# Kernel tuning notes

Measured on AMD Instinct MI355X. Metric: run time of the kernel, lower is better.

## Reference

```python
import jax, jax.numpy as jnp
import numpy as np

B, S, I, H = 16, 2048, 1024, 1024

def setup_inputs() -> dict:
    key = jax.random.key(0)
    ks = jax.random.split(key, 6)
    scale_ih = 1.0 / np.sqrt(I)
    scale_hh = 1.0 / np.sqrt(H)
    return {
        "x": jax.random.normal(ks[0], (B, S, I), dtype=jnp.float32),
        "hx": jax.random.normal(ks[1], (B, H), dtype=jnp.float32),
        "W_ih": jax.random.normal(ks[2], (H, I), dtype=jnp.float32) * scale_ih,
        "W_hh": jax.random.normal(ks[3], (H, H), dtype=jnp.float32) * scale_hh,
        "b_ih": jax.random.normal(ks[4], (H,), dtype=jnp.float32) * scale_ih,
        "b_hh": jax.random.normal(ks[5], (H,), dtype=jnp.float32) * scale_hh,
    }

def reference(x, hx, W_ih, W_hh, b_ih, b_hh):
    # Faithful to RecurrentCellWrapper: the Python loop passes the SAME
    # initial hx to the cell at every timestep (hx is never updated),
    # so all steps are independent and fully vectorizable.
    # cell: h' = tanh(x_t @ W_ih^T + b_ih + hx @ W_hh^T + b_hh)
    h_term = hx @ W_hh.T + b_hh + b_ih            # [B, H], shared across steps
    x_term = jnp.einsum('bsi,hi->bsh', x, W_ih)   # [B, S, H]
    out = jnp.tanh(x_term + h_term[:, None, :])   # [B, S, H]
    # batch_first=True: output already [batch, seq, hidden]
    return out
```

## Files before the change

kernel.cpp:

```cpp
#include <hip/hip_runtime.h>
#include <hip/hip_bf16.h>
#include <stdint.h>


#define M_TOT 32768
#define N_TOT 1024
#define K_TOT 1024

typedef short short8 __attribute__((ext_vector_type(8)));
typedef float f32x4  __attribute__((ext_vector_type(4)));

#define WS_XBF_OFF   0
#define WS_WBF_OFF   67108864
#define WS_HT_OFF    69206016

__device__ __forceinline__ unsigned short f32_to_bf16_rne(float f) {
    union { float f; unsigned int u; } v; v.f = f;
    unsigned int u = v.u;
    unsigned int r = u + 0x7fffu + ((u >> 16) & 1u);
    return (unsigned short)(r >> 16);
}

__device__ __forceinline__ float fast_tanh(float z) {
    float e = __expf(2.0f * z);
    return 1.0f - 2.0f / (e + 1.0f);
}

__global__ void convert_kernel(const float* __restrict__ x,
                               const float* __restrict__ wih,
                               unsigned short* __restrict__ xbf,
                               unsigned short* __restrict__ wbf) {
    const int NXV = 33554432 / 8;
    const int NWV = 1048576 / 8;
    int stride = gridDim.x * blockDim.x;
    for (int v = blockIdx.x * blockDim.x + threadIdx.x; v < NXV + NWV; v += stride) {
        const float* src; unsigned short* dst; long long base;
        if (v < NXV) { src = x;   dst = xbf; base = (long long)v * 8; }
        else         { src = wih; dst = wbf; base = (long long)(v - NXV) * 8; }
        float4 a = *(const float4*)(src + base);
        float4 b = *(const float4*)(src + base + 4);
        union { unsigned short s[8]; uint4 u; } o;
        o.s[0] = f32_to_bf16_rne(a.x); o.s[1] = f32_to_bf16_rne(a.y);
        o.s[2] = f32_to_bf16_rne(a.z); o.s[3] = f32_to_bf16_rne(a.w);
        o.s[4] = f32_to_bf16_rne(b.x); o.s[5] = f32_to_bf16_rne(b.y);
        o.s[6] = f32_to_bf16_rne(b.z); o.s[7] = f32_to_bf16_rne(b.w);
        *(uint4*)(dst + base) = o.u;
    }
}

__global__ void hterm_kernel(const float* __restrict__ hx,
                             const float* __restrict__ whh,
                             const float* __restrict__ bih,
                             const float* __restrict__ bhh,
                             float* __restrict__ ht) {
    int lane = threadIdx.x & 63;
    int w    = threadIdx.x >> 6;
    int wg   = blockIdx.x * 4 + w;
    int b = wg >> 10, h = wg & 1023;
    const float* hr = hx  + (long long)b * 1024;
    const float* wr = whh + (long long)h * 1024;
    float s = 0.f;
#pragma unroll
    for (int p = 0; p < 4; ++p) {
        int idx = p * 256 + lane * 4;
        float4 a = *(const float4*)(hr + idx);
        float4 c = *(const float4*)(wr + idx);
        s += a.x * c.x + a.y * c.y + a.z * c.z + a.w * c.w;
    }
#pragma unroll
    for (int d = 32; d > 0; d >>= 1) s += __shfl_down(s, d, 64);
    if (lane == 0) ht[wg] = s + bih[h] + bhh[h];
}

#define GLDS16(gp, lp) \
    __builtin_amdgcn_global_load_lds((const __attribute__((address_space(1))) void*)(gp), \
                                     (__attribute__((address_space(3))) void*)(lp), 16, 0, 0)

__global__ __launch_bounds__(256) void gemm_tanh_kernel(
    const unsigned short* __restrict__ A,
    const unsigned short* __restrict__ Bm,
    const float* __restrict__ ht,
    float* __restrict__ out)
{
    __shared__ __align__(16) char lds[16384];

    const int tid = threadIdx.x;
    const int w = tid >> 6, l = tid & 63;
    const int bid = blockIdx.x;
    const int tile_n = bid & 7;
    const int tile_m = bid >> 3;
    const int m0 = tile_m << 7, n0 = tile_n << 7;

    const int r0 = (w * 2 + 0) * 16 + (l >> 2);
    const int r1 = (w * 2 + 1) * 16 + (l >> 2);
    const int slot = l & 3;
    const int qg0 = (slot - (r0 >> 1)) & 3;
    const int qg1 = (slot - (r1 >> 1)) & 3;
    const unsigned short* gA0 = A  + (long long)(m0 + r0) * K_TOT + qg0 * 8;
    const unsigned short* gA1 = A  + (long long)(m0 + r1) * K_TOT + qg1 * 8;
    const unsigned short* gB0 = Bm + (long long)(n0 + r0) * K_TOT + qg0 * 8;
    const unsigned short* gB1 = Bm + (long long)(n0 + r1) * K_TOT + qg1 * 8;
    char* ldsA0 = lds + (w * 2 + 0) * 1024;
    char* ldsA1 = lds + (w * 2 + 1) * 1024;
    char* ldsB0 = lds + 8192 + (w * 2 + 0) * 1024;
    char* ldsB1 = lds + 8192 + (w * 2 + 1) * 1024;

    const int wm = w & 1, wn = w >> 1;
    const int lm = l & 15, q = l >> 4;
    int offA[4], offB[4];
#pragma unroll
    for (int t = 0; t < 4; ++t) {
        int rr = wm * 64 + t * 16 + lm;
        offA[t] = rr * 64 + (((q + (rr >> 1)) & 3) << 4);
        int nn = wn * 64 + t * 16 + lm;
        offB[t] = 8192 + nn * 64 + (((q + (nn >> 1)) & 3) << 4);
    }

    f32x4 acc[4][4];
#pragma unroll
    for (int i = 0; i < 4; ++i)
#pragma unroll
        for (int j = 0; j < 4; ++j)
            acc[i][j] = (f32x4){0.f, 0.f, 0.f, 0.f};

    for (int k0 = 0; k0 < K_TOT; k0 += 32) {
        GLDS16(gA0 + k0, ldsA0);
        GLDS16(gA1 + k0, ldsA1);
        GLDS16(gB0 + k0, ldsB0);
        GLDS16(gB1 + k0, ldsB1);
        __syncthreads();

        short8 af[4], bf[4];
#pragma unroll
        for (int t = 0; t < 4; ++t) {
            af[t] = *(const short8*)(lds + offA[t]);
            bf[t] = *(const short8*)(lds + offB[t]);
        }
#pragma unroll
        for (int mt = 0; mt < 4; ++mt)
#pragma unroll
            for (int nt = 0; nt < 4; ++nt)
                acc[mt][nt] = __builtin_amdgcn_mfma_f32_16x16x32_bf16(
                    af[mt], bf[nt], acc[mt][nt], 0, 0, 0);
        __syncthreads();
    }

    const int b = tile_m >> 4;
    float htv[4];
#pragma unroll
    for (int nt = 0; nt < 4; ++nt)
        htv[nt] = ht[b * 1024 + n0 + wn * 64 + nt * 16 + lm];

#pragma unroll
    for (int mt = 0; mt < 4; ++mt) {
#pragma unroll
        for (int nt = 0; nt < 4; ++nt) {
            int n = n0 + wn * 64 + nt * 16 + lm;
#pragma unroll
            for (int r = 0; r < 4; ++r) {
                int m = m0 + wm * 64 + mt * 16 + q * 4 + r;
                float z = acc[mt][nt][r] + htv[nt];
                out[(long long)m * N_TOT + n] = fast_tanh(z);
            }
        }
    }
}

extern "C" void kernel_launch(void* const* d_in, const int* in_sizes, int n_in,
                              void* d_out, int out_size, void* d_ws, size_t ws_size,
                              hipStream_t stream) {
    const float* x    = (const float*)d_in[0];
    const float* hx   = (const float*)d_in[1];
    const float* wih  = (const float*)d_in[2];
    const float* whh  = (const float*)d_in[3];
    const float* bih  = (const float*)d_in[4];
    const float* bhh  = (const float*)d_in[5];
    float* out = (float*)d_out;

    unsigned short* xbf = (unsigned short*)((char*)d_ws + WS_XBF_OFF);
    unsigned short* wbf = (unsigned short*)((char*)d_ws + WS_WBF_OFF);
    float*          htp = (float*)((char*)d_ws + WS_HT_OFF);

    hterm_kernel<<<4096, 256, 0, stream>>>(hx, whh, bih, bhh, htp);
    convert_kernel<<<2048, 256, 0, stream>>>(x, wih, xbf, wbf);
    gemm_tanh_kernel<<<2048, 256, 0, stream>>>(xbf, wbf, htp, out);
}
```

Baseline: 346.4 us.

## Fuse x bf16 conversion into GEMM A-load and merge prep kernels

```diff
diff --git a/kernel.cpp b/kernel.cpp
--- a/kernel.cpp
+++ b/kernel.cpp
@@ -10,9 +10,8 @@
 typedef short short8 __attribute__((ext_vector_type(8)));
 typedef float f32x4  __attribute__((ext_vector_type(4)));
 
-#define WS_XBF_OFF   0
-#define WS_WBF_OFF   67108864
-#define WS_HT_OFF    69206016
+#define WS_WBF_OFF 0
+#define WS_HT_OFF  2097152
 
 __device__ __forceinline__ unsigned short f32_to_bf16_rne(float f) {
     union { float f; unsigned int u; } v; v.f = f;
@@ -21,55 +20,56 @@
     return (unsigned short)(r >> 16);
 }
 
+__device__ __forceinline__ unsigned int cvt_pk_bf16(float lo, float hi) {
+    unsigned int r;
+    asm("v_cvt_pk_bf16_f32 %0, %1, %2" : "=v"(r) : "v"(lo), "v"(hi));
+    return r;
+}
+
 __device__ __forceinline__ float fast_tanh(float z) {
     float e = __expf(2.0f * z);
     return 1.0f - 2.0f / (e + 1.0f);
 }
 
-__global__ void convert_kernel(const float* __restrict__ x,
-                               const float* __restrict__ wih,
-                               unsigned short* __restrict__ xbf,
-                               unsigned short* __restrict__ wbf) {
-    const int NXV = 33554432 / 8;
-    const int NWV = 1048576 / 8;
-    int stride = gridDim.x * blockDim.x;
-    for (int v = blockIdx.x * blockDim.x + threadIdx.x; v < NXV + NWV; v += stride) {
-        const float* src; unsigned short* dst; long long base;
-        if (v < NXV) { src = x;   dst = xbf; base = (long long)v * 8; }
-        else         { src = wih; dst = wbf; base = (long long)(v - NXV) * 8; }
-        float4 a = *(const float4*)(src + base);
-        float4 b = *(const float4*)(src + base + 4);
-        union { unsigned short s[8]; uint4 u; } o;
-        o.s[0] = f32_to_bf16_rne(a.x); o.s[1] = f32_to_bf16_rne(a.y);
-        o.s[2] = f32_to_bf16_rne(a.z); o.s[3] = f32_to_bf16_rne(a.w);
-        o.s[4] = f32_to_bf16_rne(b.x); o.s[5] = f32_to_bf16_rne(b.y);
-        o.s[6] = f32_to_bf16_rne(b.z); o.s[7] = f32_to_bf16_rne(b.w);
-        *(uint4*)(dst + base) = o.u;
-    }
-}
-
-__global__ void hterm_kernel(const float* __restrict__ hx,
-                             const float* __restrict__ whh,
-                             const float* __restrict__ bih,
-                             const float* __restrict__ bhh,
-                             float* __restrict__ ht) {
-    int lane = threadIdx.x & 63;
-    int w    = threadIdx.x >> 6;
-    int wg   = blockIdx.x * 4 + w;
-    int b = wg >> 10, h = wg & 1023;
-    const float* hr = hx  + (long long)b * 1024;
-    const float* wr = whh + (long long)h * 1024;
-    float s = 0.f;
-#pragma unroll
-    for (int p = 0; p < 4; ++p) {
-        int idx = p * 256 + lane * 4;
-        float4 a = *(const float4*)(hr + idx);
-        float4 c = *(const float4*)(wr + idx);
-        s += a.x * c.x + a.y * c.y + a.z * c.z + a.w * c.w;
-    }
-#pragma unroll
-    for (int d = 32; d > 0; d >>= 1) s += __shfl_down(s, d, 64);
-    if (lane == 0) ht[wg] = s + bih[h] + bhh[h];
+__global__ void prep_kernel(const float* __restrict__ hx,
+                            const float* __restrict__ whh,
+                            const float* __restrict__ bih,
+                            const float* __restrict__ bhh,
+                            const float* __restrict__ wih,
+                            float* __restrict__ ht,
+                            unsigned short* __restrict__ wbf) {
+    if (blockIdx.x < 4096) {
+        int lane = threadIdx.x & 63;
+        int w    = threadIdx.x >> 6;
+        int wg   = blockIdx.x * 4 + w;
+        int b = wg >> 10, h = wg & 1023;
+        const float* hr = hx  + (long long)b * 1024;
+        const float* wr = whh + (long long)h * 1024;
+        float s = 0.f;
+#pragma unroll
+        for (int p = 0; p < 4; ++p) {
+            int idx = p * 256 + lane * 4;
+            float4 a = *(const float4*)(hr + idx);
+            float4 c = *(const float4*)(wr + idx);
+            s += a.x * c.x + a.y * c.y + a.z * c.z + a.w * c.w;
+        }
+#pragma unroll
+        for (int d = 32; d > 0; d >>= 1) s += __shfl_down(s, d, 64);
+        if (lane == 0) ht[wg] = s + bih[h] + bhh[h];
+    } else {
+        int g = (blockIdx.x - 4096) * 256 + threadIdx.x;
+        for (int v = g; v < 131072; v += 32768) {
+            long long base = (long long)v * 8;
+            float4 a = *(const float4*)(wih + base);
+            float4 b = *(const float4*)(wih + base + 4);
+            union { unsigned short s[8]; uint4 u; } o;
+            o.s[0] = f32_to_bf16_rne(a.x); o.s[1] = f32_to_bf16_rne(a.y);
+            o.s[2] = f32_to_bf16_rne(a.z); o.s[3] = f32_to_bf16_rne(a.w);
+            o.s[4] = f32_to_bf16_rne(b.x); o.s[5] = f32_to_bf16_rne(b.y);
+            o.s[6] = f32_to_bf16_rne(b.z); o.s[7] = f32_to_bf16_rne(b.w);
+            *(uint4*)(wbf + base) = o.u;
+        }
+    }
 }
 
 #define GLDS16(gp, lp) \
@@ -77,7 +77,7 @@
                                      (__attribute__((address_space(3))) void*)(lp), 16, 0, 0)
 
 __global__ __launch_bounds__(256) void gemm_tanh_kernel(
-    const unsigned short* __restrict__ A,
+    const float* __restrict__ X,
     const unsigned short* __restrict__ Bm,
     const float* __restrict__ ht,
     float* __restrict__ out)
@@ -86,22 +86,27 @@
 
     const int tid = threadIdx.x;
     const int w = tid >> 6, l = tid & 63;
-    const int bid = blockIdx.x;
-    const int tile_n = bid & 7;
-    const int tile_m = bid >> 3;
+
+    const int bid  = blockIdx.x;
+    const int widx = (bid & 7) * 256 + (bid >> 3);
+    const int tile_m = widx >> 3;
+    const int tile_n = widx & 7;
     const int m0 = tile_m << 7, n0 = tile_n << 7;
+
+    const int rowA  = tid >> 1;
+    const int halfA = tid & 1;
+    const float* gA = X + (long long)(m0 + rowA) * K_TOT + halfA * 16;
+    const int swzA = (rowA >> 1) & 3;
+    char* lA0 = lds + rowA * 64 + (((halfA * 2 + 0 + swzA) & 3) << 4);
+    char* lA1 = lds + rowA * 64 + (((halfA * 2 + 1 + swzA) & 3) << 4);
 
     const int r0 = (w * 2 + 0) * 16 + (l >> 2);
     const int r1 = (w * 2 + 1) * 16 + (l >> 2);
     const int slot = l & 3;
     const int qg0 = (slot - (r0 >> 1)) & 3;
     const int qg1 = (slot - (r1 >> 1)) & 3;
-    const unsigned short* gA0 = A  + (long long)(m0 + r0) * K_TOT + qg0 * 8;
-    const unsigned short* gA1 = A  + (long long)(m0 + r1) * K_TOT + qg1 * 8;
     const unsigned short* gB0 = Bm + (long long)(n0 + r0) * K_TOT + qg0 * 8;
     const unsigned short* gB1 = Bm + (long long)(n0 + r1) * K_TOT + qg1 * 8;
-    char* ldsA0 = lds + (w * 2 + 0) * 1024;
-    char* ldsA1 = lds + (w * 2 + 1) * 1024;
     char* ldsB0 = lds + 8192 + (w * 2 + 0) * 1024;
     char* ldsB1 = lds + 8192 + (w * 2 + 1) * 1024;
 
@@ -123,9 +128,19 @@
         for (int j = 0; j < 4; ++j)
             acc[i][j] = (f32x4){0.f, 0.f, 0.f, 0.f};
 
+    float4 a0 = *(const float4*)(gA + 0);
+    float4 a1 = *(const float4*)(gA + 4);
+    float4 a2 = *(const float4*)(gA + 8);
+    float4 a3 = *(const float4*)(gA + 12);
+
     for (int k0 = 0; k0 < K_TOT; k0 += 32) {
-        GLDS16(gA0 + k0, ldsA0);
-        GLDS16(gA1 + k0, ldsA1);
+        uint4 pk0, pk1;
+        pk0.x = cvt_pk_bf16(a0.x, a0.y); pk0.y = cvt_pk_bf16(a0.z, a0.w);
+        pk0.z = cvt_pk_bf16(a1.x, a1.y); pk0.w = cvt_pk_bf16(a1.z, a1.w);
+        pk1.x = cvt_pk_bf16(a2.x, a2.y); pk1.y = cvt_pk_bf16(a2.z, a2.w);
+        pk1.z = cvt_pk_bf16(a3.x, a3.y); pk1.w = cvt_pk_bf16(a3.z, a3.w);
+        *(uint4*)lA0 = pk0;
+        *(uint4*)lA1 = pk1;
         GLDS16(gB0 + k0, ldsB0);
         GLDS16(gB1 + k0, ldsB1);
         __syncthreads();
@@ -136,6 +151,15 @@
             af[t] = *(const short8*)(lds + offA[t]);
             bf[t] = *(const short8*)(lds + offB[t]);
         }
+
+        if (k0 + 32 < K_TOT) {
+            const float* nA = gA + k0 + 32;
+            a0 = *(const float4*)(nA + 0);
+            a1 = *(const float4*)(nA + 4);
+            a2 = *(const float4*)(nA + 8);
+            a3 = *(const float4*)(nA + 12);
+        }
+
 #pragma unroll
         for (int mt = 0; mt < 4; ++mt)
 #pragma unroll
@@ -177,11 +201,9 @@
     const float* bhh  = (const float*)d_in[5];
     float* out = (float*)d_out;
 
-    unsigned short* xbf = (unsigned short*)((char*)d_ws + WS_XBF_OFF);
     unsigned short* wbf = (unsigned short*)((char*)d_ws + WS_WBF_OFF);
     float*          htp = (float*)((char*)d_ws + WS_HT_OFF);
 
-    hterm_kernel<<<4096, 256, 0, stream>>>(hx, whh, bih, bhh, htp);
-    convert_kernel<<<2048, 256, 0, stream>>>(x, wih, xbf, wbf);
-    gemm_tanh_kernel<<<2048, 256, 0, stream>>>(xbf, wbf, htp, out);
-}
+    prep_kernel<<<4224, 256, 0, stream>>>(hx, whh, bih, bhh, wih, htp, wbf);
+    gemm_tanh_kernel<<<2048, 256, 0, stream>>>(x, wbf, htp, out);
+}
```

New measurement: 371.4 us. 1.07x slower.

## Merge prep kernels, double GEMM K-tile to 64, and remap blocks by column

Applied to the files above, without the earlier changes.

```diff
diff --git a/kernel.cpp b/kernel.cpp
--- a/kernel.cpp
+++ b/kernel.cpp
@@ -26,50 +26,55 @@
     return 1.0f - 2.0f / (e + 1.0f);
 }
 
-__global__ void convert_kernel(const float* __restrict__ x,
-                               const float* __restrict__ wih,
-                               unsigned short* __restrict__ xbf,
-                               unsigned short* __restrict__ wbf) {
-    const int NXV = 33554432 / 8;
-    const int NWV = 1048576 / 8;
-    int stride = gridDim.x * blockDim.x;
-    for (int v = blockIdx.x * blockDim.x + threadIdx.x; v < NXV + NWV; v += stride) {
-        const float* src; unsigned short* dst; long long base;
-        if (v < NXV) { src = x;   dst = xbf; base = (long long)v * 8; }
-        else         { src = wih; dst = wbf; base = (long long)(v - NXV) * 8; }
-        float4 a = *(const float4*)(src + base);
-        float4 b = *(const float4*)(src + base + 4);
-        union { unsigned short s[8]; uint4 u; } o;
-        o.s[0] = f32_to_bf16_rne(a.x); o.s[1] = f32_to_bf16_rne(a.y);
-        o.s[2] = f32_to_bf16_rne(a.z); o.s[3] = f32_to_bf16_rne(a.w);
-        o.s[4] = f32_to_bf16_rne(b.x); o.s[5] = f32_to_bf16_rne(b.y);
-        o.s[6] = f32_to_bf16_rne(b.z); o.s[7] = f32_to_bf16_rne(b.w);
-        *(uint4*)(dst + base) = o.u;
-    }
-}
-
-__global__ void hterm_kernel(const float* __restrict__ hx,
-                             const float* __restrict__ whh,
-                             const float* __restrict__ bih,
-                             const float* __restrict__ bhh,
-                             float* __restrict__ ht) {
-    int lane = threadIdx.x & 63;
-    int w    = threadIdx.x >> 6;
-    int wg   = blockIdx.x * 4 + w;
-    int b = wg >> 10, h = wg & 1023;
-    const float* hr = hx  + (long long)b * 1024;
-    const float* wr = whh + (long long)h * 1024;
-    float s = 0.f;
-#pragma unroll
-    for (int p = 0; p < 4; ++p) {
-        int idx = p * 256 + lane * 4;
-        float4 a = *(const float4*)(hr + idx);
-        float4 c = *(const float4*)(wr + idx);
-        s += a.x * c.x + a.y * c.y + a.z * c.z + a.w * c.w;
-    }
-#pragma unroll
-    for (int d = 32; d > 0; d >>= 1) s += __shfl_down(s, d, 64);
-    if (lane == 0) ht[wg] = s + bih[h] + bhh[h];
+__global__ void prep_kernel(const float* __restrict__ x,
+                            const float* __restrict__ wih,
+                            const float* __restrict__ hx,
+                            const float* __restrict__ whh,
+                            const float* __restrict__ bih,
+                            const float* __restrict__ bhh,
+                            unsigned short* __restrict__ xbf,
+                            unsigned short* __restrict__ wbf,
+                            float* __restrict__ ht) {
+    if (blockIdx.x < 2048) {
+        const int NXV = 33554432 / 8;
+        const int NWV = 1048576 / 8;
+        const int stride = 2048 * 256;
+        for (int v = blockIdx.x * 256 + threadIdx.x; v < NXV + NWV; v += stride) {
+            const float* src; unsigned short* dst; long long base;
+            if (v < NXV) { src = x;   dst = xbf; base = (long long)v * 8; }
+            else         { src = wih; dst = wbf; base = (long long)(v - NXV) * 8; }
+            float4 a = *(const float4*)(src + base);
+            float4 b = *(const float4*)(src + base + 4);
+            union { unsigned short s[8]; uint4 u; } o;
+            o.s[0] = f32_to_bf16_rne(a.x); o.s[1] = f32_to_bf16_rne(a.y);
+            o.s[2] = f32_to_bf16_rne(a.z); o.s[3] = f32_to_bf16_rne(a.w);
+            o.s[4] = f32_to_bf16_rne(b.x); o.s[5] = f32_to_bf16_rne(b.y);
+            o.s[6] = f32_to_bf16_rne(b.z); o.s[7] = f32_to_bf16_rne(b.w);
+            *(uint4*)(dst + base) = o.u;
+        }
+    } else {
+        int lane = threadIdx.x & 63;
+        int w    = threadIdx.x >> 6;
+        int wg_base = (blockIdx.x - 2048) * 8 + w * 2;
+#pragma unroll
+        for (int d = 0; d < 2; ++d) {
+            int wg = wg_base + d;
+            int b = wg >> 10, h = wg & 1023;
+            const float* hr = hx  + (long long)b * 1024;
+            const float* wr = whh + (long long)h * 1024;
+            float s = 0.f;
+#pragma unroll
+            for (int p = 0; p < 4; ++p) {
+                int idx = p * 256 + lane * 4;
+                float4 a = *(const float4*)(hr + idx);
+                float4 c = *(const float4*)(wr + idx);
+                s += a.x * c.x + a.y * c.y + a.z * c.z + a.w * c.w;
+            }
+#pragma unroll
+            for (int dd = 32; dd > 0; dd >>= 1) s += __shfl_down(s, dd, 64);
+            if (lane == 0) ht[wg] = s + bih[h] + bhh[h];
+        }
+    }
 }
 
 #define GLDS16(gp, lp) \
@@ -82,38 +87,44 @@
     const float* __restrict__ ht,
     float* __restrict__ out)
 {
-    __shared__ __align__(16) char lds[16384];
+    __shared__ __align__(16) char lds[32768];
 
     const int tid = threadIdx.x;
     const int w = tid >> 6, l = tid & 63;
-    const int bid = blockIdx.x;
-    const int tile_n = bid & 7;
-    const int tile_m = bid >> 3;
+
+    const int bid  = blockIdx.x;
+    const int widx = (bid & 7) * 256 + (bid >> 3);
+    const int tile_m = widx >> 3;
+    const int tile_n = widx & 7;
     const int m0 = tile_m << 7, n0 = tile_n << 7;
 
-    const int r0 = (w * 2 + 0) * 16 + (l >> 2);
-    const int r1 = (w * 2 + 1) * 16 + (l >> 2);
-    const int slot = l & 3;
-    const int qg0 = (slot - (r0 >> 1)) & 3;
-    const int qg1 = (slot - (r1 >> 1)) & 3;
-    const unsigned short* gA0 = A  + (long long)(m0 + r0) * K_TOT + qg0 * 8;
-    const unsigned short* gA1 = A  + (long long)(m0 + r1) * K_TOT + qg1 * 8;
-    const unsigned short* gB0 = Bm + (long long)(n0 + r0) * K_TOT + qg0 * 8;
-    const unsigned short* gB1 = Bm + (long long)(n0 + r1) * K_TOT + qg1 * 8;
-    char* ldsA0 = lds + (w * 2 + 0) * 1024;
-    char* ldsA1 = lds + (w * 2 + 1) * 1024;
-    char* ldsB0 = lds + 8192 + (w * 2 + 0) * 1024;
-    char* ldsB1 = lds + 8192 + (w * 2 + 1) * 1024;
+    const unsigned short* gA[4];
+    const unsigned short* gB[4];
+    char* lA[4];
+    char* lB[4];
+#pragma unroll
+    for (int j = 0; j < 4; ++j) {
+        int r  = (w * 4 + j) * 8 + (l >> 3);
+        int s  = l & 7;
+        int qg = (s - ((r >> 1) & 7)) & 7;
+        gA[j] = A  + (long long)(m0 + r) * K_TOT + qg * 8;
+        gB[j] = Bm + (long long)(n0 + r) * K_TOT + qg * 8;
+        lA[j] = lds + (w * 4 + j) * 1024;
+        lB[j] = lds + 16384 + (w * 4 + j) * 1024;
+    }
 
     const int wm = w & 1, wn = w >> 1;
     const int lm = l & 15, q = l >> 4;
-    int offA[4], offB[4];
+    int offA[4][2], offB[4][2];
 #pragma unroll
     for (int t = 0; t < 4; ++t) {
-        int rr = wm * 64 + t * 16 + lm;
-        offA[t] = rr * 64 + (((q + (rr >> 1)) & 3) << 4);
-        int nn = wn * 64 + t * 16 + lm;
-        offB[t] = 8192 + nn * 64 + (((q + (nn >> 1)) & 3) << 4);
+#pragma unroll
+        for (int sh = 0; sh < 2; ++sh) {
+            int rr = wm * 64 + t * 16 + lm;
+            offA[t][sh] = rr * 128 + (((q + 4 * sh + ((rr >> 1) & 7)) & 7) << 4);
+            int nn = wn * 64 + t * 16 + lm;
+            offB[t][sh] = 16384 + nn * 128 + (((q + 4 * sh + ((nn >> 1) & 7)) & 7) << 4);
+        }
     }
 
     f32x4 acc[4][4];
@@ -123,25 +134,42 @@
         for (int j = 0; j < 4; ++j)
             acc[i][j] = (f32x4){0.f, 0.f, 0.f, 0.f};
 
-    for (int k0 = 0; k0 < K_TOT; k0 += 32) {
-        GLDS16(gA0 + k0, ldsA0);
-        GLDS16(gA1 + k0, ldsA1);
-        GLDS16(gB0 + k0, ldsB0);
-        GLDS16(gB1 + k0, ldsB1);
+    for (int k0 = 0; k0 < K_TOT; k0 += 64) {
+#pragma unroll
+        for (int j = 0; j < 4; ++j) {
+            GLDS16(gA[j] + k0, lA[j]);
+            GLDS16(gB[j] + k0, lB[j]);
+        }
         __syncthreads();
 
-        short8 af[4], bf[4];
-#pragma unroll
-        for (int t = 0; t < 4; ++t) {
-            af[t] = *(const short8*)(lds + offA[t]);
-            bf[t] = *(const short8*)(lds + offB[t]);
-        }
-#pragma unroll
-        for (int mt = 0; mt < 4; ++mt)
-#pragma unroll
-            for (int nt = 0; nt < 4; ++nt)
-                acc[mt][nt] = __builtin_amdgcn_mfma_f32_16x16x32_bf16(
-                    af[mt], bf[nt], acc[mt][nt], 0, 0, 0);
+        {
+            short8 af[4], bfr[4];
+#pragma unroll
+            for (int t = 0; t < 4; ++t) {
+                af[t]  = *(const short8*)(lds + offA[t][0]);
+                bfr[t] = *(const short8*)(lds + offB[t][0]);
+            }
+#pragma unroll
+            for (int mt = 0; mt < 4; ++mt)
+#pragma unroll
+                for (int nt = 0; nt < 4; ++nt)
+                    acc[mt][nt] = __builtin_amdgcn_mfma_f32_16x16x32_bf16(
+                        af[mt], bfr[nt], acc[mt][nt], 0, 0, 0);
+        }
+        {
+            short8 af[4], bfr[4];
+#pragma unroll
+            for (int t = 0; t < 4; ++t) {
+                af[t]  = *(const short8*)(lds + offA[t][1]);
+                bfr[t] = *(const short8*)(lds + offB[t][1]);
+            }
+#pragma unroll
+            for (int mt = 0; mt < 4; ++mt)
+#pragma unroll
+                for (int nt = 0; nt < 4; ++nt)
+                    acc[mt][nt] = __builtin_amdgcn_mfma_f32_16x16x32_bf16(
+                        af[mt], bfr[nt], acc[mt][nt], 0, 0, 0);
+        }
         __syncthreads();
     }
 
@@ -181,7 +209,6 @@
     unsigned short* wbf = (unsigned short*)((char*)d_ws + WS_WBF_OFF);
     float*          htp = (float*)((char*)d_ws + WS_HT_OFF);
 
-    hterm_kernel<<<4096, 256, 0, stream>>>(hx, whh, bih, bhh, htp);
-    convert_kernel<<<2048, 256, 0, stream>>>(x, wih, xbf, wbf);
+    prep_kernel<<<4096, 256, 0, stream>>>(x, wih, hx, whh, bih, bhh, xbf, wbf, htp);
     gemm_tanh_kernel<<<2048, 256, 0, stream>>>(xbf, wbf, htp, out);
 }
```

Measured after the change: 330.8 us. 4.5% less time.

## Double-buffer GEMM LDS loads, remap tiles, and merge prep kernels

Applied to the files above, without the earlier changes.

```diff
diff --git a/kernel.cpp b/kernel.cpp
--- a/kernel.cpp
+++ b/kernel.cpp
@@ -26,55 +26,86 @@
     return 1.0f - 2.0f / (e + 1.0f);
 }
 
-__global__ void convert_kernel(const float* __restrict__ x,
-                               const float* __restrict__ wih,
-                               unsigned short* __restrict__ xbf,
-                               unsigned short* __restrict__ wbf) {
-    const int NXV = 33554432 / 8;
-    const int NWV = 1048576 / 8;
-    int stride = gridDim.x * blockDim.x;
-    for (int v = blockIdx.x * blockDim.x + threadIdx.x; v < NXV + NWV; v += stride) {
-        const float* src; unsigned short* dst; long long base;
-        if (v < NXV) { src = x;   dst = xbf; base = (long long)v * 8; }
-        else         { src = wih; dst = wbf; base = (long long)(v - NXV) * 8; }
-        float4 a = *(const float4*)(src + base);
-        float4 b = *(const float4*)(src + base + 4);
-        union { unsigned short s[8]; uint4 u; } o;
-        o.s[0] = f32_to_bf16_rne(a.x); o.s[1] = f32_to_bf16_rne(a.y);
-        o.s[2] = f32_to_bf16_rne(a.z); o.s[3] = f32_to_bf16_rne(a.w);
-        o.s[4] = f32_to_bf16_rne(b.x); o.s[5] = f32_to_bf16_rne(b.y);
-        o.s[6] = f32_to_bf16_rne(b.z); o.s[7] = f32_to_bf16_rne(b.w);
-        *(uint4*)(dst + base) = o.u;
-    }
-}
-
-__global__ void hterm_kernel(const float* __restrict__ hx,
-                             const float* __restrict__ whh,
-                             const float* __restrict__ bih,
-                             const float* __restrict__ bhh,
-                             float* __restrict__ ht) {
-    int lane = threadIdx.x & 63;
-    int w    = threadIdx.x >> 6;
-    int wg   = blockIdx.x * 4 + w;
-    int b = wg >> 10, h = wg & 1023;
-    const float* hr = hx  + (long long)b * 1024;
-    const float* wr = whh + (long long)h * 1024;
-    float s = 0.f;
-#pragma unroll
-    for (int p = 0; p < 4; ++p) {
-        int idx = p * 256 + lane * 4;
-        float4 a = *(const float4*)(hr + idx);
-        float4 c = *(const float4*)(wr + idx);
-        s += a.x * c.x + a.y * c.y + a.z * c.z + a.w * c.w;
-    }
-#pragma unroll
-    for (int d = 32; d > 0; d >>= 1) s += __shfl_down(s, d, 64);
-    if (lane == 0) ht[wg] = s + bih[h] + bhh[h];
+__global__ void prep_kernel(const float* __restrict__ x,
+                            const float* __restrict__ wih,
+                            const float* __restrict__ hx,
+                            const float* __restrict__ whh,
+                            const float* __restrict__ bih,
+                            const float* __restrict__ bhh,
+                            unsigned short* __restrict__ xbf,
+                            unsigned short* __restrict__ wbf,
+                            float* __restrict__ ht) {
+    if (blockIdx.x < 2048) {
+        const int NXV = 33554432 / 8;
+        const int NWV = 1048576 / 8;
+        const int stride = 2048 * 256;
+        for (int v = blockIdx.x * 256 + threadIdx.x; v < NXV + NWV; v += stride) {
+            const float* src; unsigned short* dst; long long base;
+            if (v < NXV) { src = x;   dst = xbf; base = (long long)v * 8; }
+            else         { src = wih; dst = wbf; base = (long long)(v - NXV) * 8; }
+            float4 a = *(const float4*)(src + base);
+            float4 b = *(const float4*)(src + base + 4);
+            union { unsigned short s[8]; uint4 u; } o;
+            o.s[0] = f32_to_bf16_rne(a.x); o.s[1] = f32_to_bf16_rne(a.y);
+            o.s[2] = f32_to_bf16_rne(a.z); o.s[3] = f32_to_bf16_rne(a.w);
+            o.s[4] = f32_to_bf16_rne(b.x); o.s[5] = f32_to_bf16_rne(b.y);
+            o.s[6] = f32_to_bf16_rne(b.z); o.s[7] = f32_to_bf16_rne(b.w);
+            *(uint4*)(dst + base) = o.u;
+        }
+    } else {
+        int lane = threadIdx.x & 63;
+        int w    = threadIdx.x >> 6;
+        int wg_base = (blockIdx.x - 2048) * 8 + w * 2;
+#pragma unroll
+        for (int d = 0; d < 2; ++d) {
+            int wg = wg_base + d;
+            int b = wg >> 10, h = wg & 1023;
+            const float* hr = hx  + (long long)b * 1024;
+            const float* wr = whh + (long long)h * 1024;
+            float s = 0.f;
+#pragma unroll
+            for (int p = 0; p < 4; ++p) {
+                int idx = p * 256 + lane * 4;
+                float4 a = *(const float4*)(hr + idx);
+                float4 c = *(const float4*)(wr + idx);
+                s += a.x * c.x + a.y * c.y + a.z * c.z + a.w * c.w;
+            }
+#pragma unroll
+            for (int dd = 32; dd > 0; dd >>= 1) s += __shfl_down(s, dd, 64);
+            if (lane == 0) ht[wg] = s + bih[h] + bhh[h];
+        }
+    }
 }
 
 #define GLDS16(gp, lp) \
     __builtin_amdgcn_global_load_lds((const __attribute__((address_space(1))) void*)(gp), \
                                      (__attribute__((address_space(3))) void*)(lp), 16, 0, 0)
+
+#define KITER(KNEXT, P, STAGE)                                                 \
+  {                                                                            \
+    if (STAGE) {                                                               \
+      GLDS16(gA0 + (KNEXT), lA0 + ((P) ^ 1) * 16384);                          \
+      GLDS16(gA1 + (KNEXT), lA1 + ((P) ^ 1) * 16384);                          \
+      GLDS16(gB0 + (KNEXT), lB0 + ((P) ^ 1) * 16384);                          \
+      GLDS16(gB1 + (KNEXT), lB1 + ((P) ^ 1) * 16384);                          \
+    }                                                                          \
+    {                                                                          \
+      const char* lb = lds + (P) * 16384;                                      \
+      short8 af[4], bfr[4];                                                    \
+      _Pragma("unroll")                                                        \
+      for (int t4 = 0; t4 < 4; ++t4) {                                         \
+        af[t4]  = *(const short8*)(lb + offA[t4]);                             \
+        bfr[t4] = *(const short8*)(lb + offB[t4]);                             \
+      }                                                                        \
+      _Pragma("unroll")                                                        \
+      for (int mt = 0; mt < 4; ++mt)                                           \
+        _Pragma("unroll")                                                      \
+        for (int nt = 0; nt < 4; ++nt)                                         \
+          acc[mt][nt] = __builtin_amdgcn_mfma_f32_16x16x32_bf16(               \
+              af[mt], bfr[nt], acc[mt][nt], 0, 0, 0);                          \
+    }                                                                          \
+    __syncthreads();                                                           \
+  }
 
 __global__ __launch_bounds__(256) void gemm_tanh_kernel(
     const unsigned short* __restrict__ A,
@@ -82,13 +113,15 @@
     const float* __restrict__ ht,
     float* __restrict__ out)
 {
-    __shared__ __align__(16) char lds[16384];
+    __shared__ __align__(16) char lds[32768];
 
     const int tid = threadIdx.x;
     const int w = tid >> 6, l = tid & 63;
-    const int bid = blockIdx.x;
-    const int tile_n = bid & 7;
-    const int tile_m = bid >> 3;
+
+    const int bid  = blockIdx.x;
+    const int widx = (bid & 7) * 256 + (bid >> 3);
+    const int tile_m = widx >> 3;
+    const int tile_n = widx & 7;
     const int m0 = tile_m << 7, n0 = tile_n << 7;
 
     const int r0 = (w * 2 + 0) * 16 + (l >> 2);
@@ -100,10 +133,10 @@
     const unsigned short* gA1 = A  + (long long)(m0 + r1) * K_TOT + qg1 * 8;
     const unsigned short* gB0 = Bm + (long long)(n0 + r0) * K_TOT + qg0 * 8;
     const unsigned short* gB1 = Bm + (long long)(n0 + r1) * K_TOT + qg1 * 8;
-    char* ldsA0 = lds + (w * 2 + 0) * 1024;
-    char* ldsA1 = lds + (w * 2 + 1) * 1024;
-    char* ldsB0 = lds + 8192 + (w * 2 + 0) * 1024;
-    char* ldsB1 = lds + 8192 + (w * 2 + 1) * 1024;
+    char* lA0 = lds + (w * 2 + 0) * 1024;
+    char* lA1 = lds + (w * 2 + 1) * 1024;
+    char* lB0 = lds + 8192 + (w * 2 + 0) * 1024;
+    char* lB1 = lds + 8192 + (w * 2 + 1) * 1024;
 
     const int wm = w & 1, wn = w >> 1;
     const int lm = l & 15, q = l >> 4;
@@ -123,27 +156,18 @@
         for (int j = 0; j < 4; ++j)
             acc[i][j] = (f32x4){0.f, 0.f, 0.f, 0.f};
 
-    for (int k0 = 0; k0 < K_TOT; k0 += 32) {
-        GLDS16(gA0 + k0, ldsA0);
-        GLDS16(gA1 + k0, ldsA1);
-        GLDS16(gB0 + k0, ldsB0);
-        GLDS16(gB1 + k0, ldsB1);
-        __syncthreads();
-
-        short8 af[4], bf[4];
-#pragma unroll
-        for (int t = 0; t < 4; ++t) {
-            af[t] = *(const short8*)(lds + offA[t]);
-            bf[t] = *(const short8*)(lds + offB[t]);
-        }
-#pragma unroll
-        for (int mt = 0; mt < 4; ++mt)
-#pragma unroll
-            for (int nt = 0; nt < 4; ++nt)
-                acc[mt][nt] = __builtin_amdgcn_mfma_f32_16x16x32_bf16(
-                    af[mt], bf[nt], acc[mt][nt], 0, 0, 0);
-        __syncthreads();
-    }
+    GLDS16(gA0, lA0);
+    GLDS16(gA1, lA1);
+    GLDS16(gB0, lB0);
+    GLDS16(gB1, lB1);
+    __syncthreads();
+
+    for (int i = 0; i < 30; i += 2) {
+        KITER((i + 1) * 32, 0, true);
+        KITER((i + 2) * 32, 1, true);
+    }
+    KITER(31 * 32, 0, true);
+    KITER(0,       1, false);
 
     const int b = tile_m >> 4;
     float htv[4];
@@ -181,7 +205,6 @@
     unsigned short* wbf = (unsigned short*)((char*)d_ws + WS_WBF_OFF);
     float*          htp = (float*)((char*)d_ws + WS_HT_OFF);
 
-    hterm_kernel<<<4096, 256, 0, stream>>>(hx, whh, bih, bhh, htp);
-    convert_kernel<<<2048, 256, 0, stream>>>(x, wih, xbf, wbf);
+    prep_kernel<<<4096, 256, 0, stream>>>(x, wih, hx, whh, bih, bhh, xbf, wbf, htp);
     gemm_tanh_kernel<<<2048, 256, 0, stream>>>(xbf, wbf, htp, out);
 }
```

Result: faster. 330.2 us (-4.7%).
